# Performance work log

Measured on AMD Instinct MI355X. Metric: run time of the kernel, lower is better.

## Reference

```python
import jax, jax.numpy as jnp
import numpy as np

N, E, D_IN, D, L = 50000, 100000, 78, 768, 5
BN_EPS = 1e-5


def setup_inputs() -> dict:
    key = jax.random.key(0)
    ks = jax.random.split(key, 8)
    s_in = 1.0 / np.sqrt(D_IN)
    s_d = 1.0 / np.sqrt(D)
    return {
        "x": jax.random.normal(ks[0], (N, D_IN), dtype=jnp.float32),
        "edge_index": jax.random.randint(ks[1], (2, E), 0, N, dtype=jnp.int32),
        "in_w": jax.random.normal(ks[2], (D_IN, D), dtype=jnp.float32) * s_in,
        "in_b": jnp.zeros((D,), jnp.float32),
        "conv_w": jax.random.normal(ks[3], (L, D, D), dtype=jnp.float32) * s_d,
        "conv_b": jnp.zeros((L, D), jnp.float32),
        "bn_g": jnp.ones((L, D), jnp.float32),
        "bn_b": jnp.zeros((L, D), jnp.float32),
        "out_w": jax.random.normal(ks[4], (D, D), dtype=jnp.float32) * s_d,
        "out_b": jnp.zeros((D,), jnp.float32),
    }


def reference(x, edge_index, in_w, in_b, conv_w, conv_b, bn_g, bn_b, out_w, out_b):
    src, dst = edge_index[0], edge_index[1]
    # GCN symmetric normalization with self-loops: deg over dst (col), +1 for self-loop
    deg = jax.ops.segment_sum(jnp.ones((E,), x.dtype), dst, num_segments=N) + 1.0
    dinv = jax.lax.rsqrt(deg)                      # deg >= 1, always finite
    edge_norm = (dinv[src] * dinv[dst])[:, None]   # [E, 1]
    self_norm = (dinv * dinv)[:, None]             # [N, 1] self-loop coefficient

    h = x @ in_w + in_b                            # input_proj -> [N, D]
    for l in range(L):
        xw = h @ conv_w[l]                         # GCNConv linear
        agg = jax.ops.segment_sum(xw[src] * edge_norm, dst, num_segments=N)
        agg = agg + xw * self_norm + conv_b[l]     # self-loop message + bias
        # BatchNorm1d (training mode: batch stats, biased variance)
        mu = jnp.mean(agg, axis=0)
        var = jnp.mean(jnp.square(agg - mu), axis=0)
        hn = (agg - mu) * jax.lax.rsqrt(var + BN_EPS) * bn_g[l] + bn_b[l]
        h = h + jax.nn.relu(hn)                    # residual (drop_ratio=0)
    return h @ out_w + out_b
```

## Files before the change

### kernel.cpp

```cpp
#include <hip/hip_runtime.h>
#include <hip/hip_bf16.h>
#include <stdint.h>

#define NN 50000
#define EE 100000
#define DD 768
#define MP 50176
#define KIN 96
#define SCB 196

typedef _Float16 half_t;
typedef __attribute__((ext_vector_type(8))) _Float16 v8h;
typedef __attribute__((ext_vector_type(4))) float v4f;

__device__ __forceinline__ void gload16(const half_t* g, half_t* l){
  __builtin_amdgcn_global_load_lds(
      (const __attribute__((address_space(1))) unsigned int*)(g),
      (__attribute__((address_space(3))) unsigned int*)(l),
      16, 0, 0);
}

template<int MODE>
__global__ __launch_bounds__(512, 2)
void gemm256_k(const half_t* __restrict__ A,
               const half_t* __restrict__ Bt,
               const float* __restrict__ bias,
               float* __restrict__ o32,
               half_t* __restrict__ o16)
{
  constexpr int K = 768;
  constexpr int NKT = 24;
  __shared__ __align__(16) half_t lds[3*16384];

  const int nwg = gridDim.x;
  const int q = nwg >> 3, r = nwg & 7;
  const int xcd = blockIdx.x & 7, ii = blockIdx.x >> 3;
  const int L = (xcd < r ? xcd*(q+1) : r*(q+1) + (xcd-r)*q) + ii;
  const int rowb = L / 3, colb = L - rowb*3;
  const int m0 = rowb*256, n0 = colb*256;

  const int t = threadIdx.x, l = t&63, w = t>>6;
  const int wm = w>>2, wn = w&3;

  v4f acc[8][4];
  #pragma unroll
  for (int i=0;i<8;++i)
    #pragma unroll
    for (int j=0;j<4;++j){ v4f z = {0.f,0.f,0.f,0.f}; acc[i][j]=z; }

  const int strip = w*2;
  const int srow  = strip*16 + (l>>2);
  const int sch   = ((l&3) ^ ((l>>3)&3))*8;
  const half_t* Asrc = A  + (size_t)(m0 + srow)*K + sch;
  const half_t* Bsrc = Bt + (size_t)(n0 + srow)*K + sch;

  auto STAGE = [&](int kt2, int b){
    half_t* Ab = lds + b*16384;
    half_t* Bb = Ab + 8192;
    const int ko = kt2*32;
    gload16(Asrc + ko,                Ab + strip*512);
    gload16(Bsrc + ko,                Bb + strip*512);
    gload16(Asrc + ko + 16*K,         Ab + strip*512 + 512);
    gload16(Bsrc + ko + 16*K,         Bb + strip*512 + 512);
  };

  const int ra = l&15;
  const int pc = ((l>>4) ^ ((ra>>1)&3))*8;

  v8h af[2][8], bf[2][4];

  #define LOADF(s_, base_) do{                                              \
    const half_t* Ab_ = lds + (base_);                                      \
    const half_t* Bb_ = Ab_ + 8192;                                         \
    _Pragma("unroll")                                                       \
    for (int n_=0;n_<4;++n_) bf[s_][n_] = *(const v8h*)(Bb_ + (wn*64 + n_*16 + ra)*32 + pc); \
    _Pragma("unroll")                                                       \
    for (int m_=0;m_<8;++m_) af[s_][m_] = *(const v8h*)(Ab_ + (wm*128 + m_*16 + ra)*32 + pc); \
  }while(0)

  #define MFMAS(s_) do{                                                     \
    __builtin_amdgcn_s_setprio(1);                                          \
    _Pragma("unroll")                                                       \
    for (int m_=0;m_<8;++m_)                                                \
      _Pragma("unroll")                                                     \
      for (int n_=0;n_<4;++n_)                                              \
        acc[m_][n_] = __builtin_amdgcn_mfma_f32_16x16x32_f16(af[s_][m_], bf[s_][n_], acc[m_][n_], 0,0,0); \
    __builtin_amdgcn_s_setprio(0);                                          \
  }while(0)

  STAGE(0,0); STAGE(1,1); STAGE(2,2);
  asm volatile("s_waitcnt vmcnt(8)" ::: "memory");
  __builtin_amdgcn_s_barrier();
  LOADF(0, 0);
  asm volatile("s_waitcnt lgkmcnt(0)" ::: "memory");
  __builtin_amdgcn_sched_barrier(0);

  #pragma unroll
  for (int i=0;i<NKT;++i){
    const int cur = i&1, nxt = cur^1;
    if (i < NKT-1){
      if (i < NKT-2) asm volatile("s_waitcnt vmcnt(4)" ::: "memory");
      else           asm volatile("s_waitcnt vmcnt(0)" ::: "memory");
      __builtin_amdgcn_s_barrier();
      if (i+3 < NKT) STAGE(i+3, i%3);
      LOADF(nxt, ((i+1)%3)*16384);
      MFMAS(cur);
      asm volatile("s_waitcnt lgkmcnt(0)" ::: "memory");
      __builtin_amdgcn_sched_barrier(0);
    } else {
      MFMAS(cur);
    }
  }
  #undef LOADF
  #undef MFMAS

  if (MODE==2){
    float bv[4];
    #pragma unroll
    for (int n=0;n<4;++n) bv[n] = bias[n0 + wn*64 + n*16 + ra];
    #pragma unroll
    for (int m=0;m<8;++m){
      #pragma unroll
      for (int rr=0;rr<4;++rr){
        int row = m0 + wm*128 + m*16 + (l>>4)*4 + rr;
        if (row >= NN) continue;
        #pragma unroll
        for (int n=0;n<4;++n){
          int col = n0 + wn*64 + n*16 + ra;
          o32[(size_t)row*DD + col] = acc[m][n][rr] + bv[n];
        }
      }
    }
  } else {
    #pragma unroll
    for (int p=0;p<2;++p){
      __syncthreads();
      if (wm==p){
        #pragma unroll
        for (int m=0;m<8;++m)
          #pragma unroll
          for (int rr=0;rr<4;++rr){
            int rw = m*16 + (l>>4)*4 + rr;
            #pragma unroll
            for (int n=0;n<4;++n){
              int col = wn*64 + n*16 + ra;
              lds[rw*256 + (col ^ ((rw&15)<<3))] = (half_t)acc[m][n][rr];
            }
          }
      }
      __syncthreads();
      #pragma unroll
      for (int g=0; g<8; ++g){
        int rw = (t>>5) + g*16;
        int colB = (t&31)*8;
        v8h hv = *(const v8h*)(lds + rw*256 + (colB ^ ((rw&15)<<3)));
        *(v8h*)(o16 + (size_t)(m0 + p*128 + rw)*DD + n0 + colB) = hv;
      }
    }
  }
}

__global__ __launch_bounds__(256)
void gemm128_k(const half_t* __restrict__ A,
               const half_t* __restrict__ Bt,
               int K,
               const float* __restrict__ bias,
               half_t* __restrict__ o16)
{
  __shared__ __align__(16) half_t smem[128*128];
  half_t* As = smem;
  half_t* Bs = smem + 128*32;
  const int nwg = gridDim.x;
  const int q = nwg >> 3, r = nwg & 7;
  const int xcd = blockIdx.x & 7, ii = blockIdx.x >> 3;
  const int L = (xcd < r ? xcd*(q+1) : r*(q+1) + (xcd-r)*q) + ii;
  const int rowb = L / 6, colb = L - rowb*6;
  const int m0 = rowb*128, n0 = colb*128;

  const int t = threadIdx.x, l = t&63, w = t>>6;
  const int wr = w>>1, wc = w&1;
  v4f acc[4][4];
  #pragma unroll
  for (int i=0;i<4;++i)
    #pragma unroll
    for (int j=0;j<4;++j){ v4f z = {0.f,0.f,0.f,0.f}; acc[i][j]=z; }

  const int nkt = K/32;
  for (int kt=0; kt<nkt; ++kt){
    __syncthreads();
    #pragma unroll
    for (int j=0;j<2;++j){
      int br  = w*32 + j*16;
      int row = br + (l>>2);
      int ch  = (l&3) ^ ((row>>1)&3);
      gload16(A  + (size_t)(m0+row)*K + kt*32 + ch*8, As + br*32);
      gload16(Bt + (size_t)(n0+row)*K + kt*32 + ch*8, Bs + br*32);
    }
    __syncthreads();
    v8h af[4], bf[4];
    #pragma unroll
    for (int m=0;m<4;++m){
      int row = wr*64 + m*16 + (l&15);
      int ch = (l>>4) ^ ((row>>1)&3);
      af[m] = *(const v8h*)(As + row*32 + ch*8);
    }
    #pragma unroll
    for (int n=0;n<4;++n){
      int row = wc*64 + n*16 + (l&15);
      int ch = (l>>4) ^ ((row>>1)&3);
      bf[n] = *(const v8h*)(Bs + row*32 + ch*8);
    }
    #pragma unroll
    for (int m=0;m<4;++m)
      #pragma unroll
      for (int n=0;n<4;++n)
        acc[m][n] = __builtin_amdgcn_mfma_f32_16x16x32_f16(af[m], bf[n], acc[m][n], 0,0,0);
  }

  __syncthreads();
  #pragma unroll
  for (int m=0;m<4;++m){
    #pragma unroll
    for (int rr=0;rr<4;++rr){
      int row = wr*64 + m*16 + (l>>4)*4 + rr;
      #pragma unroll
      for (int n=0;n<4;++n){
        int colL = wc*64 + n*16 + (l&15);
        float v = acc[m][n][rr] + bias[n0+colL];
        int col = colL ^ (((row>>2)&3)<<4);
        smem[row*128 + col] = (half_t)v;
      }
    }
  }
  __syncthreads();
  #pragma unroll
  for (int c=0;c<8;++c){
    int row = c*16 + (t>>4);
    int colBase = (t&15)*8;
    int col = colBase ^ (((row>>2)&3)<<4);
    v8h hv = *(const v8h*)(smem + row*128 + col);
    *(v8h*)(o16 + (size_t)(m0+row)*DD + n0 + colBase) = hv;
  }
}

__global__ void k_count(const int* __restrict__ dst, int* __restrict__ cnt){
  int e = blockIdx.x*256 + threadIdx.x;
  if (e < EE) atomicAdd(&cnt[dst[e]], 1);
}
__global__ void k_dinv(const int* __restrict__ cnt, float* __restrict__ dinv){
  int i = blockIdx.x*256 + threadIdx.x;
  if (i < MP) dinv[i] = (i < NN) ? rsqrtf((float)cnt[i] + 1.0f) : 0.f;
}
__global__ void k_bsum(const int* __restrict__ cnt, int* __restrict__ bsum){
  int i = blockIdx.x*256 + threadIdx.x;
  int v = (i < NN) ? cnt[i] : 0;
  #pragma unroll
  for (int o=1;o<64;o<<=1) v += __shfl_xor(v, o);
  __shared__ int ws_[4];
  if ((threadIdx.x&63)==0) ws_[threadIdx.x>>6] = v;
  __syncthreads();
  if (threadIdx.x==0) bsum[blockIdx.x] = ws_[0]+ws_[1]+ws_[2]+ws_[3];
}
__global__ void k_btop(const int* __restrict__ bsum, int* __restrict__ boff){
  if (threadIdx.x==0){
    int run = 0;
    for (int b=0;b<SCB;++b){ boff[b] = run; run += bsum[b]; }
  }
}
__global__ void k_rowptr(const int* __restrict__ cnt, const int* __restrict__ boff,
                         int* __restrict__ rowptr, int* __restrict__ cursor){
  __shared__ int sh[256];
  int i = blockIdx.x*256 + threadIdx.x;
  int v = (i < NN) ? cnt[i] : 0;
  sh[threadIdx.x] = v; __syncthreads();
  #pragma unroll
  for (int o=1;o<256;o<<=1){
    int add = 0;
    if (threadIdx.x >= o) add = sh[threadIdx.x - o];
    __syncthreads();
    sh[threadIdx.x] += add;
    __syncthreads();
  }
  int excl = sh[threadIdx.x] - v + boff[blockIdx.x];
  if (i <= NN) rowptr[i] = excl;
  if (i < NN)  cursor[i] = excl;
}
__global__ void k_fill(const int* __restrict__ src, const int* __restrict__ dst,
                       const float* __restrict__ dinv, int* __restrict__ cursor,
                       int* __restrict__ ss, float* __restrict__ we){
  int e = blockIdx.x*256 + threadIdx.x;
  if (e < EE){
    int s = src[e], d = dst[e];
    int pos = atomicAdd(&cursor[d], 1);
    ss[pos] = s;
    we[pos] = dinv[s]*dinv[d];
  }
}
__global__ void k_x16(const float* __restrict__ x, half_t* __restrict__ x16){
  int idx = blockIdx.x*256 + threadIdx.x;
  if (idx < MP*KIN){
    int row = idx / KIN, k = idx - row*KIN;
    float v = (row < NN && k < 78) ? x[(size_t)row*78 + k] : 0.f;
    x16[idx] = (half_t)v;
  }
}
__global__ void k_tr(const float* __restrict__ src, half_t* __restrict__ dst, int K, int ldk){
  int idx = blockIdx.x*256 + threadIdx.x;
  if (idx < DD*ldk){
    int n = idx / ldk, k = idx - n*ldk;
    dst[idx] = (k < K) ? (half_t)src[(size_t)k*DD + n] : (half_t)0.f;
  }
}

__global__ __launch_bounds__(256)
void k_gather(const int* __restrict__ rowptr, const int* __restrict__ ss,
              const float* __restrict__ we, const half_t* __restrict__ xw,
              const float* __restrict__ dinv, const float* __restrict__ bias,
              half_t* __restrict__ agg16, float* __restrict__ stats){
  const int t = threadIdx.x, l = t&63, wv = t>>6;
  float b_[12];
  #pragma unroll
  for (int j=0;j<12;++j) b_[j] = bias[l + 64*j];
  float s_[12], q_[12];
  #pragma unroll
  for (int j=0;j<12;++j){ s_[j]=0.f; q_[j]=0.f; }

  for (int d = blockIdx.x*4 + wv; d < NN; d += gridDim.x*4){
    int beg = rowptr[d], end = rowptr[d+1];
    float dv = dinv[d], sn = dv*dv;
    const half_t* xr = xw + (size_t)d*DD + l;
    float a_[12];
    #pragma unroll
    for (int j=0;j<12;++j) a_[j] = fmaf(sn, (float)xr[64*j], b_[j]);
    int e = beg;
    for (; e+1 < end; e += 2){
      int sA = ss[e], sB = ss[e+1];
      float wA = we[e], wB = we[e+1];
      const half_t* xA = xw + (size_t)sA*DD + l;
      const half_t* xB = xw + (size_t)sB*DD + l;
      #pragma unroll
      for (int j=0;j<12;++j) a_[j] += wA*(float)xA[64*j] + wB*(float)xB[64*j];
    }
    if (e < end){
      int sA = ss[e]; float wA = we[e];
      const half_t* xA = xw + (size_t)sA*DD + l;
      #pragma unroll
      for (int j=0;j<12;++j) a_[j] = fmaf(wA, (float)xA[64*j], a_[j]);
    }
    half_t* ar = agg16 + (size_t)d*DD + l;
    #pragma unroll
    for (int j=0;j<12;++j) ar[64*j] = (half_t)a_[j];
    #pragma unroll
    for (int j=0;j<12;++j){ s_[j]+=a_[j]; q_[j]+=a_[j]*a_[j]; }
  }

  __shared__ float red[4][24][64];
  #pragma unroll
  for (int j=0;j<12;++j){ red[wv][j][l] = s_[j]; red[wv][12+j][l] = q_[j]; }
  __syncthreads();
  #pragma unroll
  for (int k=0;k<6;++k){
    int idx  = t + k*256;
    int slot = idx>>6, lane = idx&63;
    float v = red[0][slot][lane]+red[1][slot][lane]+red[2][slot][lane]+red[3][slot][lane];
    int off = (slot<12) ? (lane + 64*slot) : (DD + lane + 64*(slot-12));
    atomicAdd(&stats[off], v);
  }
}

__global__ void k_final(const float* __restrict__ stats, const float* __restrict__ g,
                        const float* __restrict__ b, float* __restrict__ sc, float* __restrict__ sh){
  int t = threadIdx.x;
  #pragma unroll
  for (int j=0;j<3;++j){
    int d = t + j*256;
    float mu  = stats[d]      * (1.0f/NN);
    float msq = stats[DD+d]   * (1.0f/NN);
    float var = msq - mu*mu;
    float rstd = rsqrtf(var + 1e-5f);
    float scale = rstd * g[d];
    sc[d] = scale;
    sh[d] = b[d] - mu*scale;
  }
}
__global__ void k_apply(const half_t* __restrict__ agg16, const float* __restrict__ sc,
                        const float* __restrict__ sh, half_t* __restrict__ h16){
  const int total = NN*DD/8;
  for (int i = blockIdx.x*blockDim.x + threadIdx.x; i < total; i += gridDim.x*blockDim.x){
    size_t base = (size_t)i*8;
    int col = (int)(base % DD);
    v8h a = *(const v8h*)(agg16 + base);
    v8h h = *(const v8h*)(h16 + base);
    v8h o;
    #pragma unroll
    for (int j=0;j<8;++j){
      float v = fmaxf(fmaf((float)a[j], sc[col+j], sh[col+j]), 0.f);
      o[j] = (half_t)((float)h[j] + v);
    }
    *(v8h*)(h16 + base) = o;
  }
}

extern "C" void kernel_launch(void* const* d_in, const int* in_sizes, int n_in,
                              void* d_out, int out_size, void* d_ws, size_t ws_size,
                              hipStream_t stream){
  (void)in_sizes; (void)n_in; (void)out_size; (void)ws_size;
  const float* x      = (const float*)d_in[0];
  const int*   ei     = (const int*)  d_in[1];
  const float* in_w   = (const float*)d_in[2];
  const float* in_b   = (const float*)d_in[3];
  const float* conv_w = (const float*)d_in[4];
  const float* conv_b = (const float*)d_in[5];
  const float* bn_g   = (const float*)d_in[6];
  const float* bn_b   = (const float*)d_in[7];
  const float* out_w  = (const float*)d_in[8];
  const float* out_b  = (const float*)d_in[9];
  float* out = (float*)d_out;
  const int* srcI = ei;
  const int* dstI = ei + EE;

  char* ws = (char*)d_ws; size_t off = 0;
  auto alloc = [&](size_t b)->void*{ void* p = ws + off; off += (b + 255) & ~(size_t)255; return p; };
  half_t* h16  = (half_t*)alloc((size_t)MP*DD*2);
  half_t* xw16 = (half_t*)alloc((size_t)MP*DD*2);
  half_t* agg16= (half_t*)alloc((size_t)NN*DD*2);
  half_t* x16  = (half_t*)alloc((size_t)MP*KIN*2);
  half_t* wT   = (half_t*)alloc((size_t)(DD*KIN + 6*DD*DD)*2);
  float* dinv   = (float*)alloc((size_t)MP*4);
  int*   cnt    = (int*)  alloc((size_t)MP*4);
  int*   rowptr = (int*)  alloc((size_t)(NN+1)*4);
  int*   cursor = (int*)  alloc((size_t)NN*4);
  int*   ssE    = (int*)  alloc((size_t)EE*4);
  float* weE    = (float*)alloc((size_t)EE*4);
  int*   bsum   = (int*)  alloc((size_t)SCB*4);
  int*   boff   = (int*)  alloc((size_t)SCB*4);
  float* stats  = (float*)alloc((size_t)4*DD*4);

  half_t* wTin = wT;
  half_t* wTc  = wT + DD*KIN;
  half_t* wTo  = wTc + 5*DD*DD;

  hipMemsetAsync(cnt, 0, (size_t)MP*4, stream);
  k_count<<<(EE+255)/256,256,0,stream>>>(dstI, cnt);
  k_dinv <<<(MP+255)/256,256,0,stream>>>(cnt, dinv);
  k_bsum <<<SCB,256,0,stream>>>(cnt, bsum);
  k_btop <<<1,64,0,stream>>>(bsum, boff);
  k_rowptr<<<SCB,256,0,stream>>>(cnt, boff, rowptr, cursor);
  k_fill <<<(EE+255)/256,256,0,stream>>>(srcI, dstI, dinv, cursor, ssE, weE);
  k_x16  <<<(MP*KIN+255)/256,256,0,stream>>>(x, x16);
  k_tr   <<<(DD*KIN+255)/256,256,0,stream>>>(in_w, wTin, 78, KIN);
  for (int l = 0; l < 5; ++l)
    k_tr <<<(DD*DD+255)/256,256,0,stream>>>(conv_w + (size_t)l*DD*DD, wTc + (size_t)l*DD*DD, DD, DD);
  k_tr   <<<(DD*DD+255)/256,256,0,stream>>>(out_w, wTo, DD, DD);

  const int NWG1 = (MP/128)*(DD/128);
  gemm128_k<<<NWG1,256,0,stream>>>(x16, wTin, KIN, in_b, h16);

  const int NWG2 = (MP/256)*(DD/256);
  for (int l = 0; l < 5; ++l){
    gemm256_k<1><<<NWG2,512,0,stream>>>(h16, wTc + (size_t)l*DD*DD, nullptr, nullptr, xw16);
    hipMemsetAsync(stats, 0, (size_t)2*DD*4, stream);
    k_gather<<<2048,256,0,stream>>>(rowptr, ssE, weE, xw16, dinv, conv_b + l*DD, agg16, stats);
    k_final<<<1,256,0,stream>>>(stats, bn_g + l*DD, bn_b + l*DD, stats+2*DD, stats+3*DD);
    k_apply<<<2048,256,0,stream>>>(agg16, stats+2*DD, stats+3*DD, h16);
  }

  gemm256_k<2><<<NWG2,512,0,stream>>>(h16, wTo, out_b, out, nullptr);
}
```

Measured before the change: 1.170 ms.

## Replace 256x256 GEMM tiles with templated 128x128 pipelined kernel for all GEMMs

Turns the 512-thread 256x256-tile GEMM into a 256-thread 128x128-tile kernel templated on K, with a triple-buffered LDS pipeline and three workgroups per CU. The same kernel now also handles the K=96 input projection, replacing the simpler unpipelined gemm128 kernel. Smaller tiles mean more workgroups (better load balance across CUs for M=50176) and more occupancy, at the cost of lower arithmetic intensity per tile and more global/LDS traffic for operand reuse.

```diff
diff --git a/kernel.cpp b/kernel.cpp
--- a/kernel.cpp
+++ b/kernel.cpp
@@ -20,68 +20,67 @@
       16, 0, 0);
 }
 
-template<int MODE>
-__global__ __launch_bounds__(512, 2)
-void gemm256_k(const half_t* __restrict__ A,
-               const half_t* __restrict__ Bt,
-               const float* __restrict__ bias,
-               float* __restrict__ o32,
-               half_t* __restrict__ o16)
+template<int MODE, int KK>
+__global__ __launch_bounds__(256, 3)
+void gemm_t(const half_t* __restrict__ A,
+            const half_t* __restrict__ Bt,
+            const float* __restrict__ bias,
+            float* __restrict__ o32,
+            half_t* __restrict__ o16)
 {
-  constexpr int K = 768;
-  constexpr int NKT = 24;
-  __shared__ __align__(16) half_t lds[3*16384];
+  constexpr int NKT = KK/32;
+  __shared__ __align__(16) half_t lds[3*8192];
 
   const int nwg = gridDim.x;
   const int q = nwg >> 3, r = nwg & 7;
   const int xcd = blockIdx.x & 7, ii = blockIdx.x >> 3;
   const int L = (xcd < r ? xcd*(q+1) : r*(q+1) + (xcd-r)*q) + ii;
-  const int rowb = L / 3, colb = L - rowb*3;
-  const int m0 = rowb*256, n0 = colb*256;
+  const int rowb = L / 6, colb = L - rowb*6;
+  const int m0 = rowb*128, n0 = colb*128;
 
   const int t = threadIdx.x, l = t&63, w = t>>6;
-  const int wm = w>>2, wn = w&3;
-
-  v4f acc[8][4];
-  #pragma unroll
-  for (int i=0;i<8;++i)
+  const int wm = w>>1, wn = w&1;
+
+  v4f acc[4][4];
+  #pragma unroll
+  for (int i=0;i<4;++i)
     #pragma unroll
     for (int j=0;j<4;++j){ v4f z = {0.f,0.f,0.f,0.f}; acc[i][j]=z; }
 
-  const int strip = w*2;
-  const int srow  = strip*16 + (l>>2);
-  const int sch   = ((l&3) ^ ((l>>3)&3))*8;
-  const half_t* Asrc = A  + (size_t)(m0 + srow)*K + sch;
-  const half_t* Bsrc = Bt + (size_t)(n0 + srow)*K + sch;
+  const int srow = 16*w + (l>>2);
+  const int sch  = ((l&3) ^ ((l>>3)&3))*8;
+  const half_t* ApA = A  + (size_t)(m0 + srow)*KK + sch;
+  const half_t* ApB = Bt + (size_t)(n0 + srow)*KK + sch;
+  const int aoff = w*512;
 
   auto STAGE = [&](int kt2, int b){
-    half_t* Ab = lds + b*16384;
-    half_t* Bb = Ab + 8192;
+    half_t* Ab = lds + b*8192;
+    half_t* Bb = Ab + 4096;
     const int ko = kt2*32;
-    gload16(Asrc + ko,                Ab + strip*512);
-    gload16(Bsrc + ko,                Bb + strip*512);
-    gload16(Asrc + ko + 16*K,         Ab + strip*512 + 512);
-    gload16(Bsrc + ko + 16*K,         Bb + strip*512 + 512);
+    gload16(ApA + ko,                  Ab + aoff);
+    gload16(ApA + ko + (size_t)64*KK,  Ab + aoff + 2048);
+    gload16(ApB + ko,                  Bb + aoff);
+    gload16(ApB + ko + (size_t)64*KK,  Bb + aoff + 2048);
   };
 
   const int ra = l&15;
   const int pc = ((l>>4) ^ ((ra>>1)&3))*8;
 
-  v8h af[2][8], bf[2][4];
+  v8h af[2][4], bf[2][4];
 
   #define LOADF(s_, base_) do{                                              \
     const half_t* Ab_ = lds + (base_);                                      \
-    const half_t* Bb_ = Ab_ + 8192;                                         \
+    const half_t* Bb_ = Ab_ + 4096;                                         \
     _Pragma("unroll")                                                       \
     for (int n_=0;n_<4;++n_) bf[s_][n_] = *(const v8h*)(Bb_ + (wn*64 + n_*16 + ra)*32 + pc); \
     _Pragma("unroll")                                                       \
-    for (int m_=0;m_<8;++m_) af[s_][m_] = *(const v8h*)(Ab_ + (wm*128 + m_*16 + ra)*32 + pc); \
+    for (int m_=0;m_<4;++m_) af[s_][m_] = *(const v8h*)(Ab_ + (wm*64 + m_*16 + ra)*32 + pc); \
   }while(0)
 
   #define MFMAS(s_) do{                                                     \
     __builtin_amdgcn_s_setprio(1);                                          \
     _Pragma("unroll")                                                       \
-    for (int m_=0;m_<8;++m_)                                                \
+    for (int m_=0;m_<4;++m_)                                                \
       _Pragma("unroll")                                                     \
       for (int n_=0;n_<4;++n_)                                              \
         acc[m_][n_] = __builtin_amdgcn_mfma_f32_16x16x32_f16(af[s_][m_], bf[s_][n_], acc[m_][n_], 0,0,0); \
@@ -103,7 +102,7 @@
       else           asm volatile("s_waitcnt vmcnt(0)" ::: "memory");
       __builtin_amdgcn_s_barrier();
       if (i+3 < NKT) STAGE(i+3, i%3);
-      LOADF(nxt, ((i+1)%3)*16384);
+      LOADF(nxt, ((i+1)%3)*8192);
       MFMAS(cur);
       asm volatile("s_waitcnt lgkmcnt(0)" ::: "memory");
       __builtin_amdgcn_sched_barrier(0);
@@ -119,10 +118,10 @@
     #pragma unroll
     for (int n=0;n<4;++n) bv[n] = bias[n0 + wn*64 + n*16 + ra];
     #pragma unroll
-    for (int m=0;m<8;++m){
+    for (int m=0;m<4;++m){
       #pragma unroll
       for (int rr=0;rr<4;++rr){
-        int row = m0 + wm*128 + m*16 + (l>>4)*4 + rr;
+        int row = m0 + wm*64 + m*16 + (l>>4)*4 + rr;
         if (row >= NN) continue;
         #pragma unroll
         for (int n=0;n<4;++n){
@@ -132,114 +131,30 @@
       }
     }
   } else {
-    #pragma unroll
-    for (int p=0;p<2;++p){
-      __syncthreads();
-      if (wm==p){
+    __syncthreads();
+    #pragma unroll
+    for (int m=0;m<4;++m){
+      #pragma unroll
+      for (int rr=0;rr<4;++rr){
+        int row = wm*64 + m*16 + (l>>4)*4 + rr;
         #pragma unroll
-        for (int m=0;m<8;++m)
-          #pragma unroll
-          for (int rr=0;rr<4;++rr){
-            int rw = m*16 + (l>>4)*4 + rr;
-            #pragma unroll
-            for (int n=0;n<4;++n){
-              int col = wn*64 + n*16 + ra;
-              lds[rw*256 + (col ^ ((rw&15)<<3))] = (half_t)acc[m][n][rr];
-            }
-          }
+        for (int n=0;n<4;++n){
+          int col = wn*64 + n*16 + ra;
+          float v = acc[m][n][rr];
+          if (MODE==0) v += bias[n0+col];
+          int gran = (col>>3) ^ (row&7);
+          lds[row*128 + gran*8 + (col&7)] = (half_t)v;
+        }
       }
-      __syncthreads();
-      #pragma unroll
-      for (int g=0; g<8; ++g){
-        int rw = (t>>5) + g*16;
-        int colB = (t&31)*8;
-        v8h hv = *(const v8h*)(lds + rw*256 + (colB ^ ((rw&15)<<3)));
-        *(v8h*)(o16 + (size_t)(m0 + p*128 + rw)*DD + n0 + colB) = hv;
-      }
-    }
-  }
-}
-
-__global__ __launch_bounds__(256)
-void gemm128_k(const half_t* __restrict__ A,
-               const half_t* __restrict__ Bt,
-               int K,
-               const float* __restrict__ bias,
-               half_t* __restrict__ o16)
-{
-  __shared__ __align__(16) half_t smem[128*128];
-  half_t* As = smem;
-  half_t* Bs = smem + 128*32;
-  const int nwg = gridDim.x;
-  const int q = nwg >> 3, r = nwg & 7;
-  const int xcd = blockIdx.x & 7, ii = blockIdx.x >> 3;
-  const int L = (xcd < r ? xcd*(q+1) : r*(q+1) + (xcd-r)*q) + ii;
-  const int rowb = L / 6, colb = L - rowb*6;
-  const int m0 = rowb*128, n0 = colb*128;
-
-  const int t = threadIdx.x, l = t&63, w = t>>6;
-  const int wr = w>>1, wc = w&1;
-  v4f acc[4][4];
-  #pragma unroll
-  for (int i=0;i<4;++i)
-    #pragma unroll
-    for (int j=0;j<4;++j){ v4f z = {0.f,0.f,0.f,0.f}; acc[i][j]=z; }
-
-  const int nkt = K/32;
-  for (int kt=0; kt<nkt; ++kt){
+    }
     __syncthreads();
     #pragma unroll
-    for (int j=0;j<2;++j){
-      int br  = w*32 + j*16;
-      int row = br + (l>>2);
-      int ch  = (l&3) ^ ((row>>1)&3);
-      gload16(A  + (size_t)(m0+row)*K + kt*32 + ch*8, As + br*32);
-      gload16(Bt + (size_t)(n0+row)*K + kt*32 + ch*8, Bs + br*32);
-    }
-    __syncthreads();
-    v8h af[4], bf[4];
-    #pragma unroll
-    for (int m=0;m<4;++m){
-      int row = wr*64 + m*16 + (l&15);
-      int ch = (l>>4) ^ ((row>>1)&3);
-      af[m] = *(const v8h*)(As + row*32 + ch*8);
-    }
-    #pragma unroll
-    for (int n=0;n<4;++n){
-      int row = wc*64 + n*16 + (l&15);
-      int ch = (l>>4) ^ ((row>>1)&3);
-      bf[n] = *(const v8h*)(Bs + row*32 + ch*8);
-    }
-    #pragma unroll
-    for (int m=0;m<4;++m)
-      #pragma unroll
-      for (int n=0;n<4;++n)
-        acc[m][n] = __builtin_amdgcn_mfma_f32_16x16x32_f16(af[m], bf[n], acc[m][n], 0,0,0);
-  }
-
-  __syncthreads();
-  #pragma unroll
-  for (int m=0;m<4;++m){
-    #pragma unroll
-    for (int rr=0;rr<4;++rr){
-      int row = wr*64 + m*16 + (l>>4)*4 + rr;
-      #pragma unroll
-      for (int n=0;n<4;++n){
-        int colL = wc*64 + n*16 + (l&15);
-        float v = acc[m][n][rr] + bias[n0+colL];
-        int col = colL ^ (((row>>2)&3)<<4);
-        smem[row*128 + col] = (half_t)v;
-      }
-    }
-  }
-  __syncthreads();
-  #pragma unroll
-  for (int c=0;c<8;++c){
-    int row = c*16 + (t>>4);
-    int colBase = (t&15)*8;
-    int col = colBase ^ (((row>>2)&3)<<4);
-    v8h hv = *(const v8h*)(smem + row*128 + col);
-    *(v8h*)(o16 + (size_t)(m0+row)*DD + n0 + colBase) = hv;
+    for (int g=0; g<8; ++g){
+      int row = (t>>4) + g*16;
+      int gran = t&15;
+      v8h hv = *(const v8h*)(lds + row*128 + ((gran ^ (row&7)))*8);
+      *(v8h*)(o16 + (size_t)(m0+row)*DD + n0 + gran*8) = hv;
+    }
   }
 }
 
@@ -453,17 +368,16 @@
     k_tr <<<(DD*DD+255)/256,256,0,stream>>>(conv_w + (size_t)l*DD*DD, wTc + (size_t)l*DD*DD, DD, DD);
   k_tr   <<<(DD*DD+255)/256,256,0,stream>>>(out_w, wTo, DD, DD);
 
-  const int NWG1 = (MP/128)*(DD/128);
-  gemm128_k<<<NWG1,256,0,stream>>>(x16, wTin, KIN, in_b, h16);
-
-  const int NWG2 = (MP/256)*(DD/256);
+  const int NWG = (MP/128)*(DD/128);
+  gemm_t<0,KIN><<<NWG,256,0,stream>>>(x16, wTin, in_b, nullptr, h16);
+
   for (int l = 0; l < 5; ++l){
-    gemm256_k<1><<<NWG2,512,0,stream>>>(h16, wTc + (size_t)l*DD*DD, nullptr, nullptr, xw16);
+    gemm_t<1,DD><<<NWG,256,0,stream>>>(h16, wTc + (size_t)l*DD*DD, nullptr, nullptr, xw16);
     hipMemsetAsync(stats, 0, (size_t)2*DD*4, stream);
     k_gather<<<2048,256,0,stream>>>(rowptr, ssE, weE, xw16, dinv, conv_b + l*DD, agg16, stats);
     k_final<<<1,256,0,stream>>>(stats, bn_g + l*DD, bn_b + l*DD, stats+2*DD, stats+3*DD);
     k_apply<<<2048,256,0,stream>>>(agg16, stats+2*DD, stats+3*DD, h16);
   }
 
-  gemm256_k<2><<<NWG2,512,0,stream>>>(h16, wTo, out_b, out, nullptr);
-}
+  gemm_t<2,DD><<<NWG,256,0,stream>>>(h16, wTo, out_b, out, nullptr);
+}
```

New measurement: 1.140 ms. 2.5% less time.
